# Kernel tuning notes

Hardware: AMD Instinct MI355X
Metric: run time of the kernel (lower is better)

## Reference

```python
import jax, jax.numpy as jnp
import numpy as np

N, E, G = 50000, 800000, 64          # nodes, edges, graphs in batch
F, HG, HL = 64, 128, 128             # node feat, graph hidden, lin hidden
AVG_LOG = float(np.log(9.0))         # from deg histogram [0]*8+[1]: log(8+1)


def setup_inputs() -> dict:
    key = jax.random.key(0)
    ks = jax.random.split(key, 24)
    def w(k, shape):
        return 0.1 * jax.random.normal(k, shape, jnp.float32)
    return {
        "x": jax.random.normal(ks[0], (N, F), jnp.float32),
        "edge_index": jax.random.randint(ks[1], (2, E), 0, N),
        "edge_attr": jax.random.normal(ks[2], (E, 1), jnp.float32),
        "batch": jnp.sort(jax.random.randint(ks[3], (N,), 0, G)),
        # PNAConv params (towers=1, pre_layers=1, post_layers=1, edge_dim=1)
        "W_edge": w(ks[4], (1, F)),      "b_edge": w(ks[5], (F,)),
        "W_pre": w(ks[6], (3 * F, F)),   "b_pre": w(ks[7], (F,)),
        "W_post": w(ks[8], (13 * F, HG)), "b_post": w(ks[9], (HG,)),
        "W_lin": w(ks[10], (HG, HG)),    "b_lin": w(ks[11], (HG,)),
        # bn1 / fc2 / bn2
        "g1": jnp.ones((HG,)), "be1": jnp.zeros((HG,)),
        "W2": w(ks[12], (HG, HL)), "b2": w(ks[13], (HL,)),
        "g2": jnp.ones((HL,)), "be2": jnp.zeros((HL,)),
        # one resnet block: fc/bn/fc/bn
        "Wr1": w(ks[14], (HL, HL)), "br1": w(ks[15], (HL,)),
        "gr1": jnp.ones((HL,)), "ber1": jnp.zeros((HL,)),
        "Wr2": w(ks[16], (HL, HL)), "br2": w(ks[17], (HL,)),
        "gr2": jnp.ones((HL,)), "ber2": jnp.zeros((HL,)),
        "W_out": w(ks[18], (HL, 1)), "b_out": w(ks[19], (1,)),
    }


def _bn(z, g, b):
    # BatchNorm1d, training mode: biased batch stats, eps=1e-5
    mu = z.mean(0)
    var = ((z - mu) ** 2).mean(0)
    return (z - mu) * jax.lax.rsqrt(var + 1e-5) * g + b


def _pna(x, edge_index, edge_attr, W_edge, b_edge, W_pre, b_pre,
         W_post, b_post, W_lin, b_lin):
    src, dst = edge_index[0], edge_index[1]  # messages flow j->i, aggregate at dst
    e = edge_attr @ W_edge + b_edge                               # [E, F]
    m = jnp.concatenate([x[dst], x[src], e], -1) @ W_pre + b_pre  # [E, F]
    ones_e = jnp.ones((m.shape[0],), m.dtype)
    cnt = jax.ops.segment_sum(ones_e, dst, N)                     # in-degree
    cnt1 = jnp.maximum(cnt, 1.0)
    mean = jax.ops.segment_sum(m, dst, N) / cnt1[:, None]
    mean2 = jax.ops.segment_sum(m * m, dst, N) / cnt1[:, None]
    std = jnp.sqrt(jax.nn.relu(mean2 - mean * mean) + 1e-5)
    has = (cnt > 0)[:, None]
    mn = jnp.where(has, jax.ops.segment_min(m, dst, N), 0.0)
    mx = jnp.where(has, jax.ops.segment_max(m, dst, N), 0.0)
    agg = jnp.concatenate([mean, mn, mx, std], -1)                # [N, 4F]
    amp = (jnp.log(cnt1 + 1.0) / AVG_LOG)[:, None]                # amplification scaler
    out = jnp.concatenate([agg, agg * amp, agg / amp], -1)        # [N, 12F]
    out = jnp.concatenate([x, out], -1) @ W_post + b_post         # [N, HG]
    return out @ W_lin + b_lin                                    # [N, HG]


def reference(x, edge_index, edge_attr, batch,
              W_edge, b_edge, W_pre, b_pre, W_post, b_post, W_lin, b_lin,
              g1, be1, W2, b2, g2, be2,
              Wr1, br1, gr1, ber1, Wr2, br2, gr2, ber2,
              W_out, b_out):
    h = _pna(x, edge_index, edge_attr, W_edge, b_edge, W_pre, b_pre,
             W_post, b_post, W_lin, b_lin)
    # global_mean_pool over graphs
    gc = jnp.maximum(jax.ops.segment_sum(jnp.ones((h.shape[0],), h.dtype), batch, G), 1.0)
    z = jax.ops.segment_sum(h, batch, G) / gc[:, None]            # [G, HG]
    z = jax.nn.relu(_bn(z, g1, be1))
    z = jax.nn.relu(_bn(z @ W2 + b2, g2, be2))
    r = z
    z = jax.nn.relu(_bn(z @ Wr1 + br1, gr1, ber1))
    z = jax.nn.relu(_bn(z @ Wr2 + br2, gr2, ber2) + r)
    return z @ W_out + b_out                                      # [G, 1]
```

## Files before the change

### kernel.cpp

```cpp
#include <hip/hip_runtime.h>
#include <hip/hip_bf16.h>

using bf16 = __hip_bfloat16;

#define F 64
#define HG 128
#define HL 128
#define AVG_LOG_INV 0.45511961331341866f
#define BSH 4
#define BNODES 16
#define BCAP 512
#define BTILE 8192
#define NBMAX 3200
#define NBTMAX 128

typedef short short8 __attribute__((ext_vector_type(8)));
typedef float floatx4 __attribute__((ext_vector_type(4)));

__device__ __forceinline__ float b2f(bf16 v) { return __bfloat162float(v); }
__device__ __forceinline__ bf16 f2b(float v) { return __float2bfloat16(v); }
__device__ __forceinline__ short f2bs(float v) { bf16 h = f2b(v); return *(short*)&h; }

__device__ __forceinline__ unsigned packbf2(float x, float y) {
    bf16 a = f2b(x), b = f2b(y);
    unsigned short ua = *(unsigned short*)&a, ub = *(unsigned short*)&b;
    return ((unsigned)ub << 16) | (unsigned)ua;
}

__device__ __forceinline__ float wave_sum(float v) {
    #pragma unroll
    for (int m = 32; m > 0; m >>= 1) v += __shfl_xor(v, m);
    return v;
}

__global__ __launch_bounds__(512) void k_prep(
    const float* __restrict__ x, const float* __restrict__ W_pre,
    bf16* __restrict__ AB, int N,
    const int* __restrict__ ei, const float* __restrict__ ea,
    int* __restrict__ ofs, int2* __restrict__ gout, int E,
    float* __restrict__ gfeat, int* __restrict__ gcnt,
    int NB, int GF, int G, int NBT,
    const float* __restrict__ W_edge, const float* __restrict__ b_edge,
    const float* __restrict__ b_pre, float* __restrict__ uc) {
    __shared__ __align__(16) char smem[2 * NBMAX * 4];
    int t = threadIdx.x;
    int gtid = blockIdx.x * 512 + t;
    int gstr = gridDim.x * 512;
    for (int i = gtid; i < GF; i += gstr) gfeat[i] = 0.f;
    for (int i = gtid; i < G; i += gstr) gcnt[i] = 0;

    if (blockIdx.x < NBT) {
        int* hist = (int*)smem;
        int* aux  = hist + NBMAX;
        int p = blockIdx.x;
        for (int i = t; i < NB; i += 512) hist[i] = 0;
        __syncthreads();
        int base = p * BTILE;
        int lim = E - base; if (lim > BTILE) lim = BTILE;
        int nq = lim >> 2;
        const int4* dst4 = (const int4*)(ei + E + base);
        for (int q = t; q < nq; q += 512) {
            int4 d = dst4[q];
            atomicAdd(&hist[d.x >> BSH], 1);
            atomicAdd(&hist[d.y >> BSH], 1);
            atomicAdd(&hist[d.z >> BSH], 1);
            atomicAdd(&hist[d.w >> BSH], 1);
        }
        for (int i = (nq << 2) + t; i < lim; i += 512)
            atomicAdd(&hist[ei[E + base + i] >> BSH], 1);
        __syncthreads();
        int b0 = t * 8;
        int c[8]; int tot = 0;
        #pragma unroll
        for (int j = 0; j < 8; j++) {
            c[j] = (b0 + j < NB) ? hist[b0 + j] : 0;
            tot += c[j];
        }
        aux[t] = tot;
        __syncthreads();
        for (int d = 1; d < 512; d <<= 1) {
            int v = (t >= d) ? aux[t - d] : 0;
            __syncthreads();
            aux[t] += v;
            __syncthreads();
        }
        int run = aux[t] - tot;
        __syncthreads();
        size_t orow = (size_t)p * (NB + 1);
        #pragma unroll
        for (int j = 0; j < 8; j++) {
            if (b0 + j < NB) {
                hist[b0 + j] = run;
                ofs[orow + b0 + j] = run;
                run += c[j];
            }
        }
        if (t == 0) ofs[orow + NB] = lim;
        for (int i = t; i < NB; i += 512) aux[i] = 0;
        __syncthreads();
        const int4* src4 = (const int4*)(ei + base);
        const float4* ea4 = (const float4*)(ea + base);
        int2* seg = gout + (size_t)p * BTILE;
        for (int q = t; q < nq; q += 512) {
            int4 s = src4[q], d = dst4[q];
            float4 v = ea4[q];
            int bb, pos;
            bb = d.x >> BSH; pos = hist[bb] + atomicAdd(&aux[bb], 1);
            seg[pos] = make_int2((d.x << 16) | s.x, __float_as_int(v.x));
            bb = d.y >> BSH; pos = hist[bb] + atomicAdd(&aux[bb], 1);
            seg[pos] = make_int2((d.y << 16) | s.y, __float_as_int(v.y));
            bb = d.z >> BSH; pos = hist[bb] + atomicAdd(&aux[bb], 1);
            seg[pos] = make_int2((d.z << 16) | s.z, __float_as_int(v.z));
            bb = d.w >> BSH; pos = hist[bb] + atomicAdd(&aux[bb], 1);
            seg[pos] = make_int2((d.w << 16) | s.w, __float_as_int(v.w));
        }
        for (int i = (nq << 2) + t; i < lim; i += 512) {
            int s = ei[base + i], d = ei[E + base + i];
            int bb = d >> BSH;
            int pos = hist[bb] + atomicAdd(&aux[bb], 1);
            seg[pos] = make_int2((d << 16) | s, __float_as_int(ea[base + i]));
        }
    } else {
        if (blockIdx.x == NBT && t < 64) {
            int f = t;
            float u = 0.f, c2 = b_pre[f];
            for (int k = 0; k < 64; k++) {
                float w3 = W_pre[(128 + k) * 64 + f];
                u += W_edge[k] * w3;
                c2 += b_edge[k] * w3;
            }
            uc[f] = u; uc[64 + f] = c2;
        }
        unsigned short* wt = (unsigned short*)smem;
        for (int idx = t; idx < 8192; idx += 512) {
            int k = idx >> 7, m = idx & 127;
            float v = W_pre[((m & 64) + k) * 64 + (m & 63)];
            wt[m * 72 + k] = (unsigned short)f2bs(v);
        }
        __syncthreads();

        int lane = t & 63;
        int row = lane & 15, quad = lane >> 4;
        int w = (blockIdx.x - NBT) * 8 + (t >> 6);
        int nwaves = (gridDim.x - NBT) * 8;
        int ntiles = (N + 15) >> 4;

        for (int tile = w; tile < ntiles; tile += nwaves) {
            int m0 = tile << 4;
            int node_a = m0 + row; if (node_a >= N) node_a = N - 1;
            short8 a[2];
            #pragma unroll
            for (int h = 0; h < 2; h++) {
                const float* xp = x + (size_t)node_a * 64 + h * 32 + quad * 8;
                floatx4 v0 = *(const floatx4*)xp;
                floatx4 v1 = *(const floatx4*)(xp + 4);
                #pragma unroll
                for (int j = 0; j < 4; j++) { a[h][j] = f2bs(v0[j]); a[h][4 + j] = f2bs(v1[j]); }
            }
            #pragma unroll
            for (int tt = 0; tt < 8; tt++) {
                int fbase = tt * 16;
                floatx4 c = {0.f, 0.f, 0.f, 0.f};
                #pragma unroll
                for (int h = 0; h < 2; h++) {
                    short8 bfr = *(const short8*)(wt + (fbase + row) * 72 + h * 32 + quad * 8);
                    c = __builtin_amdgcn_mfma_f32_16x16x32_bf16(a[h], bfr, c, 0, 0, 0);
                }
                #pragma unroll
                for (int r = 0; r < 4; r++) {
                    int node = m0 + quad * 4 + r;
                    if (node < N) AB[(size_t)node * 128 + fbase + row] = f2b(c[r]);
                }
            }
        }
    }
}

__global__ __launch_bounds__(256) void k_edge(
    const bf16* __restrict__ AB, const int2* __restrict__ gout,
    const int* __restrict__ ofs, const float* __restrict__ uc,
    const int* __restrict__ batch, const float* __restrict__ x,
    float* __restrict__ gfeat, int* __restrict__ gcnt,
    int N, int NB, int NBT) {
    __shared__ int2 recs[BCAP], sortd[BCAP];
    __shared__ int ncnt[BNODES], nofs[BNODES], nrank[BNODES];
    __shared__ int gid[BNODES];
    __shared__ unsigned lstat[BNODES][128];
    __shared__ float lamp[BNODES], liamp[BNODES];
    __shared__ int runlo[NBTMAX], runpre[NBTMAX];
    __shared__ int etot_s;
    int t = threadIdx.x;
    int b = blockIdx.x;
    int nn = N - b * BNODES; if (nn > BNODES) nn = BNODES;

    if (t < 64) {
        int l = t;
        int p0 = 2 * l, p1 = 2 * l + 1;
        int lo0 = 0, len0 = 0, lo1 = 0, len1 = 0;
        if (p0 < NBT) {
            lo0 = ofs[(size_t)p0 * (NB + 1) + b];
            len0 = ofs[(size_t)p0 * (NB + 1) + b + 1] - lo0;
        }
        if (p1 < NBT) {
            lo1 = ofs[(size_t)p1 * (NB + 1) + b];
            len1 = ofs[(size_t)p1 * (NB + 1) + b + 1] - lo1;
        }
        runlo[p0] = lo0; runlo[p1] = lo1;
        int s = len0 + len1, inc = s;
        #pragma unroll
        for (int m = 1; m < 64; m <<= 1) { int u = __shfl_up(inc, m); if (l >= m) inc += u; }
        int ex = inc - s;
        runpre[p0] = ex; runpre[p1] = ex + len0;
        if (l == 63) etot_s = inc;
    } else if (t < 64 + BNODES) {
        int i = t - 64;
        ncnt[i] = 0; nrank[i] = 0;
        if (i < nn) gid[i] = batch[b * BNODES + i];
    }
    __syncthreads();

    int ecnt = etot_s; if (ecnt > BCAP) ecnt = BCAP;
    for (int i = t; i < ecnt; i += 256) {
        int lo2 = 0, hi2 = NBTMAX;
        while (hi2 - lo2 > 1) {
            int mid = (lo2 + hi2) >> 1;
            if (runpre[mid] <= i) lo2 = mid; else hi2 = mid;
        }
        int2 r = gout[(size_t)lo2 * BTILE + runlo[lo2] + (i - runpre[lo2])];
        recs[i] = r;
        atomicAdd(&ncnt[((unsigned)r.x >> 16) & (BNODES - 1)], 1);
    }
    __syncthreads();
    if (t < BNODES) {
        int v = ncnt[t], inc = v;
        #pragma unroll
        for (int m = 1; m < BNODES; m <<= 1) { int u = __shfl_up(inc, m); if (t >= m) inc += u; }
        nofs[t] = inc - v;
    }
    __syncthreads();
    for (int i = t; i < ecnt; i += 256) {
        int2 r = recs[i];
        int nl = ((unsigned)r.x >> 16) & (BNODES - 1);
        int k = atomicAdd(&nrank[nl], 1);
        sortd[nofs[nl] + k] = r;
    }
    __syncthreads();

    int lane = t & 63, w = t >> 6;
    int half = lane & 31, hi32 = lane >> 5;
    float2 u2 = *(const float2*)(uc + 2 * half);
    float2 c2 = *(const float2*)(uc + 64 + 2 * half);

    for (int nl = w; nl < nn; nl += 8) {
        int nlA = nl, nlB = nl + 4;
        bool hasB = (nlB < nn);
        int nA = b * BNODES + nlA;
        int nB = b * BNODES + (hasB ? nlB : nlA);
        int loA = nofs[nlA], cntA = ncnt[nlA];
        int loB = hasB ? nofs[nlB] : 0, cntB = hasB ? ncnt[nlB] : 0;

        unsigned apA = *(const unsigned*)(AB + (size_t)nA * 128 + 2 * half);
        unsigned apB = *(const unsigned*)(AB + (size_t)nB * 128 + 2 * half);
        float acxA = __uint_as_float(apA << 16) + c2.x;
        float acyA = __uint_as_float(apA & 0xffff0000u) + c2.y;
        float acxB = __uint_as_float(apB << 16) + c2.x;
        float acyB = __uint_as_float(apB & 0xffff0000u) + c2.y;

        float sxA = 0.f, syA = 0.f, qxA = 0.f, qyA = 0.f;
        float mnxA = 3.4e38f, mnyA = 3.4e38f, mxxA = -3.4e38f, mxyA = -3.4e38f;
        float sxB = 0.f, syB = 0.f, qxB = 0.f, qyB = 0.f;
        float mnxB = 3.4e38f, mnyB = 3.4e38f, mxxB = -3.4e38f, mxyB = -3.4e38f;

        auto gaddr = [&](int sn) {
            return (const unsigned*)(AB + (size_t)sn * 128 + 64 + 2 * half);
        };

        for (int i = hi32; (i < cntA) || (i < cntB); i += 8) {
            unsigned bpA[4], bpB[4];
            #pragma unroll
            for (int j = 0; j < 4; j++) {
                int idx = i + 2 * j;
                int e = loA + (idx < cntA ? idx : 0);
                bpA[j] = *gaddr(sortd[e].x & 0xFFFF);
            }
            #pragma unroll
            for (int j = 0; j < 4; j++) {
                int idx = i + 2 * j;
                int e = loB + (idx < cntB ? idx : 0);
                bpB[j] = *gaddr(sortd[e].x & 0xFFFF);
            }
            #pragma unroll
            for (int j = 0; j < 4; j++) {
                int idx = i + 2 * j;
                if (idx < cntA) {
                    float eav = __int_as_float(sortd[loA + idx].y);
                    float bx = __uint_as_float(bpA[j] << 16);
                    float by = __uint_as_float(bpA[j] & 0xffff0000u);
                    float m0 = fmaf(eav, u2.x, acxA) + bx;
                    float m1 = fmaf(eav, u2.y, acyA) + by;
                    sxA += m0; qxA = fmaf(m0, m0, qxA);
                    syA += m1; qyA = fmaf(m1, m1, qyA);
                    mnxA = fminf(mnxA, m0); mxxA = fmaxf(mxxA, m0);
                    mnyA = fminf(mnyA, m1); mxyA = fmaxf(mxyA, m1);
                }
            }
            #pragma unroll
            for (int j = 0; j < 4; j++) {
                int idx = i + 2 * j;
                if (idx < cntB) {
                    float eav = __int_as_float(sortd[loB + idx].y);
                    float bx = __uint_as_float(bpB[j] << 16);
                    float by = __uint_as_float(bpB[j] & 0xffff0000u);
                    float m0 = fmaf(eav, u2.x, acxB) + bx;
                    float m1 = fmaf(eav, u2.y, acyB) + by;
                    sxB += m0; qxB = fmaf(m0, m0, qxB);
                    syB += m1; qyB = fmaf(m1, m1, qyB);
                    mnxB = fminf(mnxB, m0); mxxB = fmaxf(mxxB, m0);
                    mnyB = fminf(mnyB, m1); mxyB = fmaxf(mxyB, m1);
                }
            }
        }

        auto finish = [&](int nl_, int cnt, float sx, float sy, float qx, float qy,
                          float mnx, float mny, float mxx, float mxy) {
            sx += __shfl_xor(sx, 32); sy += __shfl_xor(sy, 32);
            qx += __shfl_xor(qx, 32); qy += __shfl_xor(qy, 32);
            mnx = fminf(mnx, __shfl_xor(mnx, 32)); mny = fminf(mny, __shfl_xor(mny, 32));
            mxx = fmaxf(mxx, __shfl_xor(mxx, 32)); mxy = fmaxf(mxy, __shfl_xor(mxy, 32));
            float c1 = (cnt > 0) ? (float)cnt : 1.f;
            float inv = 1.f / c1;
            float mex = sx * inv, mey = sy * inv;
            float vx = qx * inv - mex * mex; if (vx < 0.f) vx = 0.f;
            float vy = qy * inv - mey * mey; if (vy < 0.f) vy = 0.f;
            float sdx = sqrtf(vx + 1e-5f), sdy = sqrtf(vy + 1e-5f);
            if (cnt == 0) { mnx = mny = mxx = mxy = 0.f; }
            if (hi32 == 0) {
                lstat[nl_][half]      = packbf2(mex, mey);
                lstat[nl_][32 + half] = packbf2(mnx, mny);
            } else {
                lstat[nl_][64 + half] = packbf2(mxx, mxy);
                lstat[nl_][96 + half] = packbf2(sdx, sdy);
            }
            if (lane == 0) {
                float amp = logf(c1 + 1.f) * AVG_LOG_INV;
                lamp[nl_] = amp; liamp[nl_] = 1.f / amp;
            }
        };
        finish(nlA, cntA, sxA, syA, qxA, qyA, mnxA, mnyA, mxxA, mxyA);
        if (hasB) finish(nlB, cntB, sxB, syB, qxB, qyB, mnxB, mnyB, mxxB, mxyB);
    }
    __syncthreads();

    if (t < 128) {
        int c = t;
        int elem = ((c >> 5) << 6) + ((c & 31) << 1);
        float s1x = 0.f, s1y = 0.f, s2x = 0.f, s2y = 0.f, s3x = 0.f, s3y = 0.f;
        int cur = gid[0];
        for (int nl = 0; nl < nn; nl++) {
            int g = gid[nl];
            if (g != cur) {
                float* gf = gfeat + (size_t)cur * 832;
                unsafeAtomicAdd(&gf[64 + elem], s1x);
                unsafeAtomicAdd(&gf[65 + elem], s1y);
                unsafeAtomicAdd(&gf[320 + elem], s2x);
                unsafeAtomicAdd(&gf[321 + elem], s2y);
                unsafeAtomicAdd(&gf[576 + elem], s3x);
                unsafeAtomicAdd(&gf[577 + elem], s3y);
                s1x = s1y = s2x = s2y = s3x = s3y = 0.f;
                cur = g;
            }
            unsigned p = lstat[nl][c];
            float bx = __uint_as_float(p << 16);
            float by = __uint_as_float(p & 0xffff0000u);
            float a = lamp[nl], ia = liamp[nl];
            s1x += bx; s2x = fmaf(bx, a, s2x); s3x = fmaf(bx, ia, s3x);
            s1y += by; s2y = fmaf(by, a, s2y); s3y = fmaf(by, ia, s3y);
        }
        float* gf = gfeat + (size_t)cur * 832;
        unsafeAtomicAdd(&gf[64 + elem], s1x);
        unsafeAtomicAdd(&gf[65 + elem], s1y);
        unsafeAtomicAdd(&gf[320 + elem], s2x);
        unsafeAtomicAdd(&gf[321 + elem], s2y);
        unsafeAtomicAdd(&gf[576 + elem], s3x);
        unsafeAtomicAdd(&gf[577 + elem], s3y);
    } else if (t < 192) {
        int c = t - 128;
        float sxv = 0.f;
        int cur = gid[0];
        for (int nl = 0; nl < nn; nl++) {
            int g = gid[nl];
            if (g != cur) {
                unsafeAtomicAdd(&gfeat[(size_t)cur * 832 + c], sxv);
                sxv = 0.f; cur = g;
            }
            sxv += x[(size_t)(b * BNODES + nl) * 64 + c];
        }
        unsafeAtomicAdd(&gfeat[(size_t)cur * 832 + c], sxv);
    } else if (t == 192) {
        int cnt = 0, cur = gid[0];
        for (int nl = 0; nl < nn; nl++) {
            int g = gid[nl];
            if (g != cur) { atomicAdd(&gcnt[cur], cnt); cnt = 0; cur = g; }
            cnt++;
        }
        atomicAdd(&gcnt[cur], cnt);
    }
}

__global__ void k_post1(const float* __restrict__ gfeat, const int* __restrict__ gcnt,
                        const float* __restrict__ W_post, const float* __restrict__ b_post,
                        const float* __restrict__ W_lin, const float* __restrict__ b_lin,
                        float* __restrict__ Zin) {
    int g = blockIdx.x, t = threadIdx.x;
    int j = t & 127, h = t >> 7;
    __shared__ float feat[832];
    __shared__ float part[256];
    __shared__ float z1[128];
    int cg = gcnt[g];
    float r = 1.f / ((cg > 0) ? (float)cg : 1.f);
    for (int i = t; i < 832; i += 256) feat[i] = gfeat[(size_t)g * 832 + i] * r;
    __syncthreads();
    float acc = (h == 0) ? b_post[j] : 0.f;
    const float* Wp = W_post + (size_t)(h * 416) * 128 + j;
    const float* fp = feat + h * 416;
    #pragma unroll 8
    for (int k = 0; k < 416; k++) acc += fp[k] * Wp[(size_t)k * 128];
    part[t] = acc;
    __syncthreads();
    if (t < 128) z1[j] = part[j] + part[128 + j];
    __syncthreads();
    float a2 = (h == 0) ? b_lin[j] : 0.f;
    #pragma unroll
    for (int k = 0; k < 64; k++) a2 += z1[h * 64 + k] * W_lin[(h * 64 + k) * 128 + j];
    part[t] = a2;
    __syncthreads();
    if (t < 128) {
        float v = part[j] + part[128 + j];
        if (cg == 0) v = 0.f;
        Zin[g * 128 + j] = v;
    }
}

__global__ void k_mlpcol(const float* __restrict__ in, const float* __restrict__ W,
                         const float* __restrict__ bias,
                         const float* __restrict__ gamma, const float* __restrict__ beta,
                         const float* __restrict__ res,
                         const float* __restrict__ g_in, const float* __restrict__ be_in,
                         float* __restrict__ outp) {
    __shared__ float A[64 * 129];
    __shared__ float part[4 * 64];
    int t = threadIdx.x;
    int j = blockIdx.x;

    for (int i = t; i < 8192; i += 256) A[(i >> 7) * 129 + (i & 127)] = in[i];
    __syncthreads();

    if (g_in) {
        if (t < 128) {
            int c = t;
            float mu = 0.f;
            for (int r = 0; r < 64; r++) mu += A[r * 129 + c];
            mu *= (1.f / 64.f);
            float var = 0.f;
            for (int r = 0; r < 64; r++) { float d = A[r * 129 + c] - mu; var += d * d; }
            var *= (1.f / 64.f);
            float sc = rsqrtf(var + 1e-5f) * g_in[c], sh = be_in[c];
            for (int r = 0; r < 64; r++) {
                float v = (A[r * 129 + c] - mu) * sc + sh;
                A[r * 129 + c] = v > 0.f ? v : 0.f;
            }
        }
        __syncthreads();
    }

    int r = t & 63, q = t >> 6;
    float acc = 0.f;
    int k0 = q * 32;
    #pragma unroll
    for (int k = 0; k < 32; k++) acc += A[r * 129 + k0 + k] * W[(k0 + k) * 128 + j];
    part[q * 64 + r] = acc;
    __syncthreads();

    if (t < 64) {
        float v = part[t] + part[64 + t] + part[128 + t] + part[192 + t] + bias[j];
        float mu = wave_sum(v) * (1.f / 64.f);
        float d = v - mu;
        float var = wave_sum(d * d) * (1.f / 64.f);
        float o = d * rsqrtf(var + 1e-5f) * gamma[j] + beta[j];
        if (res) o += res[t * 128 + j];
        outp[t * 128 + j] = o > 0.f ? o : 0.f;
    }
}

__global__ void k_out(const float* __restrict__ z4, const float* __restrict__ W_out,
                      const float* b_out, float* __restrict__ out) {
    int g = threadIdx.x;
    float acc = b_out[0];
    for (int j = 0; j < 128; j++) acc += z4[g * 128 + j] * W_out[j];
    out[g] = acc;
}

extern "C" void kernel_launch(void* const* d_in, const int* in_sizes, int n_in,
                              void* d_out, int out_size, void* d_ws, size_t ws_size,
                              hipStream_t stream) {
    const float* x      = (const float*)d_in[0];
    const int*   ei     = (const int*)d_in[1];
    const float* ea     = (const float*)d_in[2];
    const int*   batch  = (const int*)d_in[3];
    const float* W_edge = (const float*)d_in[4];
    const float* b_edge = (const float*)d_in[5];
    const float* W_pre  = (const float*)d_in[6];
    const float* b_pre  = (const float*)d_in[7];
    const float* W_post = (const float*)d_in[8];
    const float* b_post = (const float*)d_in[9];
    const float* W_lin  = (const float*)d_in[10];
    const float* b_lin  = (const float*)d_in[11];
    const float* g1     = (const float*)d_in[12];
    const float* be1    = (const float*)d_in[13];
    const float* W2     = (const float*)d_in[14];
    const float* b2     = (const float*)d_in[15];
    const float* g2     = (const float*)d_in[16];
    const float* be2    = (const float*)d_in[17];
    const float* Wr1    = (const float*)d_in[18];
    const float* br1    = (const float*)d_in[19];
    const float* gr1    = (const float*)d_in[20];
    const float* ber1   = (const float*)d_in[21];
    const float* Wr2    = (const float*)d_in[22];
    const float* br2    = (const float*)d_in[23];
    const float* gr2    = (const float*)d_in[24];
    const float* ber2   = (const float*)d_in[25];
    const float* W_out  = (const float*)d_in[26];
    const float* b_out  = (const float*)d_in[27];
    float* out = (float*)d_out;

    const int N = in_sizes[0] / F;
    const int E = in_sizes[1] / 2;
    const int G = out_size;
    const int NB = (N + BNODES - 1) >> BSH;

    char* p = (char*)d_ws;
    auto alloc = [&](size_t nbytes) { void* r = p; p += (nbytes + 255) & ~(size_t)255; return r; };
    const int NBT = (E + BTILE - 1) / BTILE;
    bf16*  AB     = (bf16*)alloc((size_t)N * 128 * sizeof(bf16));
    int2*  gout   = (int2*)alloc((size_t)NBT * BTILE * sizeof(int2));
    int*   ofs    = (int*)alloc((size_t)NBT * (NB + 1) * sizeof(int));
    float* uc     = (float*)alloc(128 * sizeof(float));
    float* gfeat  = (float*)alloc((size_t)G * 832 * sizeof(float));
    int*   gcnt   = (int*)alloc((size_t)G * sizeof(int));
    float* Zin    = (float*)alloc(64 * 128 * sizeof(float));
    float* z2b    = (float*)alloc(64 * 128 * sizeof(float));
    float* z3b    = (float*)alloc(64 * 128 * sizeof(float));
    float* z4b    = (float*)alloc(64 * 128 * sizeof(float));

    const int GF = G * 832;
    const int NAB = (((N + 15) >> 4) + 7) >> 3;

    k_prep<<<NBT + NAB, 512, 0, stream>>>(x, W_pre, AB, N, ei, ea, ofs, gout, E,
                                          gfeat, gcnt, NB, GF, G, NBT,
                                          W_edge, b_edge, b_pre, uc);
    k_edge<<<NB, 256, 0, stream>>>(AB, gout, ofs, uc, batch, x, gfeat, gcnt, N, NB, NBT);
    k_post1<<<G, 256, 0, stream>>>(gfeat, gcnt, W_post, b_post, W_lin, b_lin, Zin);
    k_mlpcol<<<HG, 256, 0, stream>>>(Zin, W2, b2, g2, be2, nullptr, g1, be1, z2b);
    k_mlpcol<<<HL, 256, 0, stream>>>(z2b, Wr1, br1, gr1, ber1, nullptr, nullptr, nullptr, z3b);
    k_mlpcol<<<HL, 256, 0, stream>>>(z3b, Wr2, br2, gr2, ber2, z2b, nullptr, nullptr, z4b);
    k_out<<<1, 64, 0, stream>>>(z4b, W_out, b_out, out);
}
```

Before: 223.5 us.

## Use larger edge bucket tiles and widen post-projection kernel to 1024 threads

The edge-bucketing tile grows from 8192 to 32768 records. That cuts the number of tiles from up to 128 to at most 32, so each node block scans fewer runs and the prefix scan shrinks to one 32-lane pass. The post-aggregation projection kernel now launches 1024 threads per graph and splits the 832-long and 128-long reductions eight ways, which shortens the serial dependent loops. The trade-off is a larger reduction over partial sums and fewer, bigger prep blocks.

```diff
diff --git a/kernel.cpp b/kernel.cpp
--- a/kernel.cpp
+++ b/kernel.cpp
@@ -10,9 +10,9 @@
 #define BSH 4
 #define BNODES 16
 #define BCAP 512
-#define BTILE 8192
+#define BTILE 32768
 #define NBMAX 3200
-#define NBTMAX 128
+#define NBTMAX 32
 
 typedef short short8 __attribute__((ext_vector_type(8)));
 typedef float floatx4 __attribute__((ext_vector_type(4)));
@@ -195,23 +195,17 @@
 
     if (t < 64) {
         int l = t;
-        int p0 = 2 * l, p1 = 2 * l + 1;
-        int lo0 = 0, len0 = 0, lo1 = 0, len1 = 0;
-        if (p0 < NBT) {
-            lo0 = ofs[(size_t)p0 * (NB + 1) + b];
-            len0 = ofs[(size_t)p0 * (NB + 1) + b + 1] - lo0;
-        }
-        if (p1 < NBT) {
-            lo1 = ofs[(size_t)p1 * (NB + 1) + b];
-            len1 = ofs[(size_t)p1 * (NB + 1) + b + 1] - lo1;
-        }
-        runlo[p0] = lo0; runlo[p1] = lo1;
-        int s = len0 + len1, inc = s;
+        int lo0 = 0, len0 = 0;
+        if (l < NBT) {
+            lo0 = ofs[(size_t)l * (NB + 1) + b];
+            len0 = ofs[(size_t)l * (NB + 1) + b + 1] - lo0;
+        }
+        if (l < NBTMAX) runlo[l] = lo0;
+        int inc = len0;
         #pragma unroll
-        for (int m = 1; m < 64; m <<= 1) { int u = __shfl_up(inc, m); if (l >= m) inc += u; }
-        int ex = inc - s;
-        runpre[p0] = ex; runpre[p1] = ex + len0;
-        if (l == 63) etot_s = inc;
+        for (int m = 1; m < 32; m <<= 1) { int u = __shfl_up(inc, m); if ((l & 31) >= m) inc += u; }
+        if (l < NBTMAX) runpre[l] = inc - len0;
+        if (l == 31) etot_s = inc;
     } else if (t < 64 + BNODES) {
         int i = t - 64;
         ncnt[i] = 0; nrank[i] = 0;
@@ -407,35 +401,43 @@
     }
 }
 
-__global__ void k_post1(const float* __restrict__ gfeat, const int* __restrict__ gcnt,
-                        const float* __restrict__ W_post, const float* __restrict__ b_post,
-                        const float* __restrict__ W_lin, const float* __restrict__ b_lin,
-                        float* __restrict__ Zin) {
+__global__ __launch_bounds__(1024) void k_post1(
+    const float* __restrict__ gfeat, const int* __restrict__ gcnt,
+    const float* __restrict__ W_post, const float* __restrict__ b_post,
+    const float* __restrict__ W_lin, const float* __restrict__ b_lin,
+    float* __restrict__ Zin) {
     int g = blockIdx.x, t = threadIdx.x;
     int j = t & 127, h = t >> 7;
     __shared__ float feat[832];
-    __shared__ float part[256];
+    __shared__ float part[1024];
     __shared__ float z1[128];
     int cg = gcnt[g];
     float r = 1.f / ((cg > 0) ? (float)cg : 1.f);
-    for (int i = t; i < 832; i += 256) feat[i] = gfeat[(size_t)g * 832 + i] * r;
+    for (int i = t; i < 832; i += 1024) feat[i] = gfeat[(size_t)g * 832 + i] * r;
     __syncthreads();
     float acc = (h == 0) ? b_post[j] : 0.f;
-    const float* Wp = W_post + (size_t)(h * 416) * 128 + j;
-    const float* fp = feat + h * 416;
+    const float* Wp = W_post + (size_t)(h * 104) * 128 + j;
+    const float* fp = feat + h * 104;
     #pragma unroll 8
-    for (int k = 0; k < 416; k++) acc += fp[k] * Wp[(size_t)k * 128];
+    for (int k = 0; k < 104; k++) acc += fp[k] * Wp[(size_t)k * 128];
     part[t] = acc;
     __syncthreads();
-    if (t < 128) z1[j] = part[j] + part[128 + j];
+    if (t < 128) {
+        float s = 0.f;
+        #pragma unroll
+        for (int hh = 0; hh < 8; hh++) s += part[hh * 128 + j];
+        z1[j] = s;
+    }
     __syncthreads();
     float a2 = (h == 0) ? b_lin[j] : 0.f;
     #pragma unroll
-    for (int k = 0; k < 64; k++) a2 += z1[h * 64 + k] * W_lin[(h * 64 + k) * 128 + j];
+    for (int k = 0; k < 16; k++) a2 += z1[h * 16 + k] * W_lin[(h * 16 + k) * 128 + j];
     part[t] = a2;
     __syncthreads();
     if (t < 128) {
-        float v = part[j] + part[128 + j];
+        float v = 0.f;
+        #pragma unroll
+        for (int hh = 0; hh < 8; hh++) v += part[hh * 128 + j];
         if (cg == 0) v = 0.f;
         Zin[g * 128 + j] = v;
     }
@@ -559,7 +561,7 @@
                                           gfeat, gcnt, NB, GF, G, NBT,
                                           W_edge, b_edge, b_pre, uc);
     k_edge<<<NB, 256, 0, stream>>>(AB, gout, ofs, uc, batch, x, gfeat, gcnt, N, NB, NBT);
-    k_post1<<<G, 256, 0, stream>>>(gfeat, gcnt, W_post, b_post, W_lin, b_lin, Zin);
+    k_post1<<<G, 1024, 0, stream>>>(gfeat, gcnt, W_post, b_post, W_lin, b_lin, Zin);
     k_mlpcol<<<HG, 256, 0, stream>>>(Zin, W2, b2, g2, be2, nullptr, g1, be1, z2b);
     k_mlpcol<<<HL, 256, 0, stream>>>(z2b, Wr1, br1, gr1, ber1, nullptr, nullptr, nullptr, z3b);
     k_mlpcol<<<HL, 256, 0, stream>>>(z3b, Wr2, br2, gr2, ber2, z2b, nullptr, nullptr, z4b);
```

Result: slower. 235.4 us (+5.3%).
